# Kernel tuning notes

Measured on AMD Instinct MI355X. Metric: run time of the kernel, lower is better.

Reference implementation:

```python
import jax, jax.numpy as jnp
import numpy as np

N_EMBD = 1024
N_HEAD = 16
HEAD_SIZE = N_EMBD // N_HEAD


def setup_inputs() -> dict:
    key = jax.random.key(0)
    k1, k2, k3, k4 = jax.random.split(key, 4)
    x = jax.random.normal(k1, (2, 2048, N_EMBD), dtype=jnp.float32)
    # nn.Linear weights: stored as [out, in]; apply as x @ W.T
    scale = 1.0 / np.sqrt(N_EMBD)
    W_kqv = jax.random.uniform(k2, (3 * N_EMBD, N_EMBD), jnp.float32, -scale, scale)
    W_proj = jax.random.uniform(k3, (N_EMBD, N_EMBD), jnp.float32, -scale, scale)
    b_proj = jax.random.uniform(k4, (N_EMBD,), jnp.float32, -scale, scale)
    return {"x": x, "W_kqv": W_kqv, "W_proj": W_proj, "b_proj": b_proj}


def reference(x, W_kqv, W_proj, b_proj):
    B, T, C = x.shape
    H, D = N_HEAD, HEAD_SIZE
    kqv = x @ W_kqv.T  # [B, T, 3C]
    # source splits as k, q, v (k first)
    k, q, v = jnp.split(kqv, 3, axis=-1)
    k = k.reshape(B, T, H, D).transpose(0, 2, 1, 3)  # [B,H,T,D]
    q = q.reshape(B, T, H, D).transpose(0, 2, 1, 3)
    v = v.reshape(B, T, H, D).transpose(0, 2, 1, 3)
    wei = jnp.einsum('bhqd,bhkd->bhqk', q, k) * (D ** -0.5)  # [B,H,T,T]
    causal = jnp.tril(jnp.ones((T, T), dtype=bool))
    wei = jnp.where(causal[None, None], wei, -jnp.inf)
    wei = jax.nn.softmax(wei, axis=-1)
    out = jnp.einsum('bhqk,bhkd->bhqd', wei, v)  # [B,H,T,D]
    out = out.transpose(0, 2, 1, 3).reshape(B, T, C)
    return out @ W_proj.T + b_proj
```

## Files before the change

### kernel.cpp

```cpp
#include <hip/hip_runtime.h>
#include <cstdint>


typedef __bf16 bf16x8 __attribute__((ext_vector_type(8)));
typedef unsigned short u16x8 __attribute__((ext_vector_type(8)));
typedef float f32x4 __attribute__((ext_vector_type(4)));

__device__ __forceinline__ float bf2f(unsigned short u) {
    return __uint_as_float(((unsigned int)u) << 16);
}
__device__ __forceinline__ unsigned short f2bf(float f) {
    unsigned int u = __float_as_uint(f);
    u += 0x7fffu + ((u >> 16) & 1u);
    return (unsigned short)(u >> 16);
}
__device__ __forceinline__ void stC(float* p, float v) { *p = v; }
__device__ __forceinline__ void stC(unsigned short* p, float v) { *p = f2bf(v); }

__device__ __forceinline__ void gl2lds16(const unsigned short* g, unsigned short* l) {
    __builtin_amdgcn_global_load_lds(
        (__attribute__((address_space(1))) void*)g,
        (__attribute__((address_space(3))) void*)l, 16, 0, 0);
}

__device__ __forceinline__ unsigned short* swz(unsigned short* base, int row, int col) {
    const int off = ((row << 7) + (col << 1)) ^ ((row & 7) << 4);
    return (unsigned short*)((char*)base + off);
}
__device__ __forceinline__ const unsigned short* swz(const unsigned short* base, int row, int col) {
    const int off = ((row << 7) + (col << 1)) ^ ((row & 7) << 4);
    return (const unsigned short*)((const char*)base + off);
}

__device__ __forceinline__ void cvt8(const float* __restrict__ s, unsigned short* __restrict__ d) {
    const f32x4 a = *(const f32x4*)s;
    const f32x4 b = *(const f32x4*)(s + 4);
    u16x8 o;
    o[0] = f2bf(a[0]); o[1] = f2bf(a[1]); o[2] = f2bf(a[2]); o[3] = f2bf(a[3]);
    o[4] = f2bf(b[0]); o[5] = f2bf(b[1]); o[6] = f2bf(b[2]); o[7] = f2bf(b[3]);
    *(u16x8*)d = o;
}
__global__ __launch_bounds__(256) void cvt_bf16_3(
    const float* __restrict__ s0, unsigned short* __restrict__ d0, int n0,
    const float* __restrict__ s1, unsigned short* __restrict__ d1, int n1,
    const float* __restrict__ s2, unsigned short* __restrict__ d2, int n2)
{
    const int t = blockIdx.x * 256 + threadIdx.x;
    const int S = gridDim.x * 256;
    for (int i = t; i < n0 / 8; i += S) cvt8(s0 + (size_t)i * 8, d0 + (size_t)i * 8);
    for (int i = t; i < n1 / 8; i += S) cvt8(s1 + (size_t)i * 8, d1 + (size_t)i * 8);
    for (int i = t; i < n2 / 8; i += S) cvt8(s2 + (size_t)i * 8, d2 + (size_t)i * 8);
}

__global__ __launch_bounds__(256, 3) void gemm_qkv(
    const unsigned short* __restrict__ A, const unsigned short* __restrict__ B,
    unsigned short* __restrict__ C, int M, int N, int K)
{
    __shared__ __align__(16) unsigned short As[128 * 64];
    __shared__ __align__(16) unsigned short Bs[128 * 64];

    const int tid = threadIdx.x;
    const int bn = blockIdx.x, bm = blockIdx.y;
    const int w = tid >> 6, lane = tid & 63;
    const int quad = lane >> 4, l16 = lane & 15;
    const int wm = (w >> 1) * 64, wn = (w & 1) * 64;

    f32x4 acc[4][4] = {};

    const int srow = (lane >> 3);
    const int scol = ((lane & 7) ^ srow) * 8;
    const unsigned short* Ag = &A[(size_t)(bm * 128 + w * 32 + srow) * K + scol];
    const unsigned short* Bg = &B[(size_t)(bn * 128 + w * 32 + srow) * K + scol];
    unsigned short* AsW = &As[(w * 32) * 64];
    unsigned short* BsW = &Bs[(w * 32) * 64];

    for (int k0 = 0; k0 < K; k0 += 64) {
#pragma unroll
        for (int i = 0; i < 4; i++) {
            gl2lds16(Ag + (size_t)(i * 8) * K + k0, AsW + i * 8 * 64);
            gl2lds16(Bg + (size_t)(i * 8) * K + k0, BsW + i * 8 * 64);
        }
        __syncthreads();

#pragma unroll
        for (int ks = 0; ks < 2; ks++) {
            bf16x8 af[4], bfr[4];
#pragma unroll
            for (int t = 0; t < 4; t++) {
                af[t]  = *(const bf16x8*)swz(As, wm + t * 16 + l16, ks * 32 + quad * 8);
                bfr[t] = *(const bf16x8*)swz(Bs, wn + t * 16 + l16, ks * 32 + quad * 8);
            }
#pragma unroll
            for (int mt = 0; mt < 4; mt++)
#pragma unroll
                for (int nt = 0; nt < 4; nt++)
                    acc[mt][nt] = __builtin_amdgcn_mfma_f32_16x16x32_bf16(
                        af[mt], bfr[nt], acc[mt][nt], 0, 0, 0);
        }
        __syncthreads();
    }

#pragma unroll
    for (int mt = 0; mt < 4; mt++) {
        const int row = bm * 128 + wm + mt * 16 + quad * 4;
#pragma unroll
        for (int nt = 0; nt < 4; nt++) {
            const int col = bn * 128 + wn + nt * 16 + l16;
#pragma unroll
            for (int r = 0; r < 4; r++)
                stC(&C[(size_t)(row + r) * N + col], acc[mt][nt][r]);
        }
    }
}

__global__ __launch_bounds__(256) void gemm_proj(
    const unsigned short* __restrict__ A, const unsigned short* __restrict__ B,
    const float* __restrict__ bias, float* __restrict__ C, int M, int N, int K)
{
    __shared__ __align__(16) unsigned short As[64 * 32];
    __shared__ __align__(16) unsigned short Bs[128 * 32];

    const int tid = threadIdx.x;
    const int bn = blockIdx.x, bm = blockIdx.y;
    const int w = tid >> 6, lane = tid & 63;
    const int quad = lane >> 4, l16 = lane & 15;
    const int wm = (w >> 1) * 32, wn = (w & 1) * 64;

    f32x4 acc[2][4] = {};

    const int srow = w * 16 + (lane >> 2);
    const int scol = (lane & 3) * 8;
    const unsigned short* Ag = &A[(size_t)(bm * 64 + srow) * K + scol];
    const unsigned short* Bg = &B[(size_t)(bn * 128 + srow) * K + scol];
    unsigned short* AsW = &As[(w * 16) * 32];
    unsigned short* BsW = &Bs[(w * 16) * 32];

    for (int k0 = 0; k0 < K; k0 += 32) {
        gl2lds16(Ag + k0, AsW);
        gl2lds16(Bg + k0, BsW);
        gl2lds16(Bg + (size_t)64 * K + k0, BsW + 64 * 32);
        __syncthreads();

        bf16x8 af[2], bfr[4];
#pragma unroll
        for (int t = 0; t < 2; t++)
            af[t]  = *(const bf16x8*)&As[(wm + t * 16 + l16) * 32 + quad * 8];
#pragma unroll
        for (int t = 0; t < 4; t++)
            bfr[t] = *(const bf16x8*)&Bs[(wn + t * 16 + l16) * 32 + quad * 8];
#pragma unroll
        for (int mt = 0; mt < 2; mt++)
#pragma unroll
            for (int nt = 0; nt < 4; nt++)
                acc[mt][nt] = __builtin_amdgcn_mfma_f32_16x16x32_bf16(
                    af[mt], bfr[nt], acc[mt][nt], 0, 0, 0);
        __syncthreads();
    }

#pragma unroll
    for (int mt = 0; mt < 2; mt++) {
        const int row = bm * 64 + wm + mt * 16 + quad * 4;
#pragma unroll
        for (int nt = 0; nt < 4; nt++) {
            const int col = bn * 128 + wn + nt * 16 + l16;
            const float bv = bias[col];
#pragma unroll
            for (int r = 0; r < 4; r++)
                C[(size_t)(row + r) * N + col] = acc[mt][nt][r] + bv;
        }
    }
}

__global__ __launch_bounds__(256) void attn_fused(
    const unsigned short* __restrict__ kqv,
    unsigned short* __restrict__ out)
{
    __shared__ __align__(16) unsigned short Qs[64 * 64];
    __shared__ __align__(16) unsigned short Ks[2][64 * 64];
    __shared__ __align__(16) unsigned short Vts[2][64 * 64];
    __shared__ __align__(16) unsigned short Ps[64 * 64];

    const int bh = blockIdx.x;
    const int qt = 31 - (int)blockIdx.y;
    const int b = bh >> 4, h = bh & 15;
    const int tid = threadIdx.x;
    const int w = tid >> 6;
    const int lane = tid & 63;
    const int quad = lane >> 4, l16 = lane & 15;
    const int rowBase = b * 2048;
    const int kOff = h * 64, qOff = 1024 + h * 64, vOff = 2048 + h * 64;
    const float SEXP = 0.125f * 1.4426950408889634f;
    const float MASKV = -1.0e30f;

#pragma unroll
    for (int i = 0; i < 2; i++) {
        const int v = tid + i * 256;
        const int row = v >> 3, c8 = (v & 7) * 8;
        *(u16x8*)swz(Qs, row, c8) =
            *(const u16x8*)&kqv[(size_t)(rowBase + qt * 64 + row) * 3072 + qOff + c8];
    }

    f32x4 o[4] = {};
    float l_i[4] = {0.f, 0.f, 0.f, 0.f};

    u16x8 kr[2], vr[2];
#pragma unroll
    for (int i = 0; i < 2; i++) {
        const int v = tid + i * 256;
        kr[i] = *(const u16x8*)&kqv[(size_t)(rowBase + (v >> 3)) * 3072 + kOff + (v & 7) * 8];
        vr[i] = *(const u16x8*)&kqv[(size_t)(rowBase + lane) * 3072 + vOff + (i * 4 + w) * 8];
    }

    for (int j = 0; j <= qt; j++) {
        const int cur = j & 1;
#pragma unroll
        for (int i = 0; i < 2; i++) {
            const int v = tid + i * 256;
            *(u16x8*)swz(Ks[cur], v >> 3, (v & 7) * 8) = kr[i];
            const int d8 = i * 4 + w;
#pragma unroll
            for (int u = 0; u < 8; u++)
                *swz(Vts[cur], d8 * 8 + u, lane) = vr[i][u];
        }
        __syncthreads();

        if (j < qt) {
#pragma unroll
            for (int i = 0; i < 2; i++) {
                const int v = tid + i * 256;
                kr[i] = *(const u16x8*)&kqv[(size_t)(rowBase + (j + 1) * 64 + (v >> 3)) * 3072 + kOff + (v & 7) * 8];
                vr[i] = *(const u16x8*)&kqv[(size_t)(rowBase + (j + 1) * 64 + lane) * 3072 + vOff + (i * 4 + w) * 8];
            }
        }

        f32x4 s[4] = {};
#pragma unroll
        for (int ks = 0; ks < 2; ks++) {
            const bf16x8 aq = *(const bf16x8*)swz(Qs, w * 16 + l16, ks * 32 + quad * 8);
#pragma unroll
            for (int nt = 0; nt < 4; nt++) {
                const bf16x8 bk = *(const bf16x8*)swz(Ks[cur], nt * 16 + l16, ks * 32 + quad * 8);
                s[nt] = __builtin_amdgcn_mfma_f32_16x16x32_bf16(aq, bk, s[nt], 0, 0, 0);
            }
        }

        if (j == qt) {
            const int rowl = w * 16 + quad * 4;
#pragma unroll
            for (int nt = 0; nt < 4; nt++) {
                const int coll = nt * 16 + l16;
#pragma unroll
                for (int r = 0; r < 4; r++)
                    if (coll > rowl + r) s[nt][r] = MASKV;
            }
        }

#pragma unroll
        for (int nt = 0; nt < 4; nt++) {
#pragma unroll
            for (int r = 0; r < 4; r++) {
                const float p = exp2f(s[nt][r] * SEXP);
                l_i[r] += p;
                *swz(Ps, w * 16 + quad * 4 + r, nt * 16 + l16) = f2bf(p);
            }
        }
        __syncthreads();

#pragma unroll
        for (int ks = 0; ks < 2; ks++) {
            const bf16x8 ap = *(const bf16x8*)swz(Ps, w * 16 + l16, ks * 32 + quad * 8);
#pragma unroll
            for (int nt = 0; nt < 4; nt++) {
                const bf16x8 bv = *(const bf16x8*)swz(Vts[cur], nt * 16 + l16, ks * 32 + quad * 8);
                o[nt] = __builtin_amdgcn_mfma_f32_16x16x32_bf16(ap, bv, o[nt], 0, 0, 0);
            }
        }
    }

    float linv[4];
#pragma unroll
    for (int r = 0; r < 4; r++) {
        float t = l_i[r];
        t += __shfl_xor(t, 1);
        t += __shfl_xor(t, 2);
        t += __shfl_xor(t, 4);
        t += __shfl_xor(t, 8);
        linv[r] = 1.0f / t;
    }

#pragma unroll
    for (int nt = 0; nt < 4; nt++) {
        const int col = h * 64 + nt * 16 + l16;
#pragma unroll
        for (int r = 0; r < 4; r++)
            out[(size_t)(rowBase + qt * 64 + w * 16 + quad * 4 + r) * 1024 + col] =
                f2bf(o[nt][r] * linv[r]);
    }
}

extern "C" void kernel_launch(void* const* d_in, const int* in_sizes, int n_in,
                              void* d_out, int out_size, void* d_ws, size_t ws_size,
                              hipStream_t stream) {
    const float* x     = (const float*)d_in[0];
    const float* Wkqv  = (const float*)d_in[1];
    const float* Wproj = (const float*)d_in[2];
    const float* bproj = (const float*)d_in[3];
    float* out = (float*)d_out;

    unsigned short* kqv    = (unsigned short*)d_ws;
    unsigned short* attn   = kqv    + (size_t)4096 * 3072;
    unsigned short* xb     = attn   + (size_t)4096 * 1024;
    unsigned short* wkqvb  = xb     + (size_t)4096 * 1024;
    unsigned short* wprojb = wkqvb  + (size_t)3072 * 1024;

    cvt_bf16_3<<<dim3(512), dim3(256), 0, stream>>>(
        x, xb, 4096 * 1024, Wkqv, wkqvb, 3072 * 1024, Wproj, wprojb, 1024 * 1024);

    gemm_qkv<<<dim3(24, 32), dim3(256), 0, stream>>>(
        xb, wkqvb, kqv, 4096, 3072, 1024);

    attn_fused<<<dim3(32, 32), dim3(256), 0, stream>>>(kqv, attn);

    gemm_proj<<<dim3(8, 64), dim3(256), 0, stream>>>(
        attn, wprojb, bproj, out, 4096, 1024, 1024);
}
```

Measured before the change: 184.5 us.

## Process 128 query rows per attention block with 8 waves sharing K/V tiles

The attention kernel now uses 512 threads and a 128-row query tile, so each 64-row K/V tile loaded into LDS serves twice as many query rows. The grid halves along the query dimension and each thread loads one K/V vector per iteration instead of two. Waves whose rows lie entirely before a key tile skip its MFMA and softmax work but still take part in the barriers. This cuts redundant K/V global traffic, at the cost of fewer blocks, more LDS per block, and idle waves on the diagonal tiles.

After: 188.2 us. 1.02x slower.

```diff
diff --git a/kernel.cpp b/kernel.cpp
--- a/kernel.cpp
+++ b/kernel.cpp
@@ -171,17 +171,17 @@
     }
 }
 
-__global__ __launch_bounds__(256) void attn_fused(
+__global__ __launch_bounds__(512) void attn_fused(
     const unsigned short* __restrict__ kqv,
     unsigned short* __restrict__ out)
 {
-    __shared__ __align__(16) unsigned short Qs[64 * 64];
+    __shared__ __align__(16) unsigned short Qs[128 * 64];
     __shared__ __align__(16) unsigned short Ks[2][64 * 64];
     __shared__ __align__(16) unsigned short Vts[2][64 * 64];
-    __shared__ __align__(16) unsigned short Ps[64 * 64];
+    __shared__ __align__(16) unsigned short Ps[128 * 64];
 
     const int bh = blockIdx.x;
-    const int qt = 31 - (int)blockIdx.y;
+    const int qt = 15 - (int)blockIdx.y;
     const int b = bh >> 4, h = bh & 15;
     const int tid = threadIdx.x;
     const int w = tid >> 6;
@@ -191,88 +191,82 @@
     const int kOff = h * 64, qOff = 1024 + h * 64, vOff = 2048 + h * 64;
     const float SEXP = 0.125f * 1.4426950408889634f;
     const float MASKV = -1.0e30f;
+    const int jmax = 2 * qt + 1;
 
 #pragma unroll
     for (int i = 0; i < 2; i++) {
-        const int v = tid + i * 256;
+        const int v = tid + i * 512;
         const int row = v >> 3, c8 = (v & 7) * 8;
         *(u16x8*)swz(Qs, row, c8) =
-            *(const u16x8*)&kqv[(size_t)(rowBase + qt * 64 + row) * 3072 + qOff + c8];
+            *(const u16x8*)&kqv[(size_t)(rowBase + qt * 128 + row) * 3072 + qOff + c8];
     }
 
     f32x4 o[4] = {};
     float l_i[4] = {0.f, 0.f, 0.f, 0.f};
 
-    u16x8 kr[2], vr[2];
-#pragma unroll
-    for (int i = 0; i < 2; i++) {
-        const int v = tid + i * 256;
-        kr[i] = *(const u16x8*)&kqv[(size_t)(rowBase + (v >> 3)) * 3072 + kOff + (v & 7) * 8];
-        vr[i] = *(const u16x8*)&kqv[(size_t)(rowBase + lane) * 3072 + vOff + (i * 4 + w) * 8];
-    }
-
-    for (int j = 0; j <= qt; j++) {
+    u16x8 kr, vr;
+    kr = *(const u16x8*)&kqv[(size_t)(rowBase + (tid >> 3)) * 3072 + kOff + (tid & 7) * 8];
+    vr = *(const u16x8*)&kqv[(size_t)(rowBase + lane) * 3072 + vOff + w * 8];
+
+    for (int j = 0; j <= jmax; j++) {
         const int cur = j & 1;
-#pragma unroll
-        for (int i = 0; i < 2; i++) {
-            const int v = tid + i * 256;
-            *(u16x8*)swz(Ks[cur], v >> 3, (v & 7) * 8) = kr[i];
-            const int d8 = i * 4 + w;
-#pragma unroll
-            for (int u = 0; u < 8; u++)
-                *swz(Vts[cur], d8 * 8 + u, lane) = vr[i][u];
-        }
-        __syncthreads();
-
-        if (j < qt) {
-#pragma unroll
-            for (int i = 0; i < 2; i++) {
-                const int v = tid + i * 256;
-                kr[i] = *(const u16x8*)&kqv[(size_t)(rowBase + (j + 1) * 64 + (v >> 3)) * 3072 + kOff + (v & 7) * 8];
-                vr[i] = *(const u16x8*)&kqv[(size_t)(rowBase + (j + 1) * 64 + lane) * 3072 + vOff + (i * 4 + w) * 8];
-            }
-        }
-
-        f32x4 s[4] = {};
-#pragma unroll
-        for (int ks = 0; ks < 2; ks++) {
-            const bf16x8 aq = *(const bf16x8*)swz(Qs, w * 16 + l16, ks * 32 + quad * 8);
+        *(u16x8*)swz(Ks[cur], tid >> 3, (tid & 7) * 8) = kr;
+#pragma unroll
+        for (int u = 0; u < 8; u++)
+            *swz(Vts[cur], w * 8 + u, lane) = vr[u];
+        __syncthreads();
+
+        if (j < jmax) {
+            kr = *(const u16x8*)&kqv[(size_t)(rowBase + (j + 1) * 64 + (tid >> 3)) * 3072 + kOff + (tid & 7) * 8];
+            vr = *(const u16x8*)&kqv[(size_t)(rowBase + (j + 1) * 64 + lane) * 3072 + vOff + w * 8];
+        }
+
+        const bool skip = (j << 6) > (qt * 128 + w * 16 + 15);
+        if (!skip) {
+            f32x4 s[4] = {};
+#pragma unroll
+            for (int ks = 0; ks < 2; ks++) {
+                const bf16x8 aq = *(const bf16x8*)swz(Qs, w * 16 + l16, ks * 32 + quad * 8);
+#pragma unroll
+                for (int nt = 0; nt < 4; nt++) {
+                    const bf16x8 bk = *(const bf16x8*)swz(Ks[cur], nt * 16 + l16, ks * 32 + quad * 8);
+                    s[nt] = __builtin_amdgcn_mfma_f32_16x16x32_bf16(aq, bk, s[nt], 0, 0, 0);
+                }
+            }
+
+            const int qg = qt * 128 + w * 16 + quad * 4;
+            const int kbase = j << 6;
+            if (kbase + 63 > qg) {
+#pragma unroll
+                for (int nt = 0; nt < 4; nt++) {
+                    const int kcol = kbase + nt * 16 + l16;
+#pragma unroll
+                    for (int r = 0; r < 4; r++)
+                        if (kcol > qg + r) s[nt][r] = MASKV;
+                }
+            }
+
 #pragma unroll
             for (int nt = 0; nt < 4; nt++) {
-                const bf16x8 bk = *(const bf16x8*)swz(Ks[cur], nt * 16 + l16, ks * 32 + quad * 8);
-                s[nt] = __builtin_amdgcn_mfma_f32_16x16x32_bf16(aq, bk, s[nt], 0, 0, 0);
-            }
-        }
-
-        if (j == qt) {
-            const int rowl = w * 16 + quad * 4;
-#pragma unroll
-            for (int nt = 0; nt < 4; nt++) {
-                const int coll = nt * 16 + l16;
-#pragma unroll
-                for (int r = 0; r < 4; r++)
-                    if (coll > rowl + r) s[nt][r] = MASKV;
-            }
-        }
-
-#pragma unroll
-        for (int nt = 0; nt < 4; nt++) {
-#pragma unroll
-            for (int r = 0; r < 4; r++) {
-                const float p = exp2f(s[nt][r] * SEXP);
-                l_i[r] += p;
-                *swz(Ps, w * 16 + quad * 4 + r, nt * 16 + l16) = f2bf(p);
-            }
-        }
-        __syncthreads();
-
-#pragma unroll
-        for (int ks = 0; ks < 2; ks++) {
-            const bf16x8 ap = *(const bf16x8*)swz(Ps, w * 16 + l16, ks * 32 + quad * 8);
-#pragma unroll
-            for (int nt = 0; nt < 4; nt++) {
-                const bf16x8 bv = *(const bf16x8*)swz(Vts[cur], nt * 16 + l16, ks * 32 + quad * 8);
-                o[nt] = __builtin_amdgcn_mfma_f32_16x16x32_bf16(ap, bv, o[nt], 0, 0, 0);
+#pragma unroll
+                for (int r = 0; r < 4; r++) {
+                    const float p = exp2f(s[nt][r] * SEXP);
+                    l_i[r] += p;
+                    *swz(Ps, w * 16 + quad * 4 + r, nt * 16 + l16) = f2bf(p);
+                }
+            }
+        }
+        __syncthreads();
+
+        if (!skip) {
+#pragma unroll
+            for (int ks = 0; ks < 2; ks++) {
+                const bf16x8 ap = *(const bf16x8*)swz(Ps, w * 16 + l16, ks * 32 + quad * 8);
+#pragma unroll
+                for (int nt = 0; nt < 4; nt++) {
+                    const bf16x8 bv = *(const bf16x8*)swz(Vts[cur], nt * 16 + l16, ks * 32 + quad * 8);
+                    o[nt] = __builtin_amdgcn_mfma_f32_16x16x32_bf16(ap, bv, o[nt], 0, 0, 0);
+                }
             }
         }
     }
@@ -293,7 +287,7 @@
         const int col = h * 64 + nt * 16 + l16;
 #pragma unroll
         for (int r = 0; r < 4; r++)
-            out[(size_t)(rowBase + qt * 64 + w * 16 + quad * 4 + r) * 1024 + col] =
+            out[(size_t)(rowBase + qt * 128 + w * 16 + quad * 4 + r) * 1024 + col] =
                 f2bf(o[nt][r] * linv[r]);
     }
 }
@@ -319,7 +313,7 @@
     gemm_qkv<<<dim3(24, 32), dim3(256), 0, stream>>>(
         xb, wkqvb, kqv, 4096, 3072, 1024);
 
-    attn_fused<<<dim3(32, 32), dim3(256), 0, stream>>>(kqv, attn);
+    attn_fused<<<dim3(32, 16), dim3(512), 0, stream>>>(kqv, attn);
 
     gemm_proj<<<dim3(8, 64), dim3(256), 0, stream>>>(
         attn, wprojb, bproj, out, 4096, 1024, 1024);
```
